# Optimization experiments

Measured on AMD Instinct MI355X. Metric: run time of the kernel, lower is better.

## Reference

```python
import jax, jax.numpy as jnp
import numpy as np

B, S, D, F, T, NS, L, H = 8, 1024, 1024, 4096, 64, 512, 32, 16
TAG_RATE = 0.5      # config.tagging_rate
GSR = 0.5           # config.gate_scaling_rate
ATT_EPS = 1e-12     # config.layer_norm_eps (att_norm)
ENC_EPS = 1e-5      # torch TransformerEncoderLayer default


def _ln(x, g, b, eps):
    m = x.mean(-1, keepdims=True)
    v = x.var(-1, keepdims=True)
    return (x - m) * jax.lax.rsqrt(v + eps) * g + b


def _rope(x):
    # standard rotary embedding over the full hidden dim
    d = x.shape[-1]
    s = x.shape[1]
    inv = 1.0 / (10000.0 ** (jnp.arange(0, d, 2, dtype=jnp.float32) / d))
    ang = jnp.arange(s, dtype=jnp.float32)[:, None] * inv[None, :]  # [S, D/2]
    sin, cos = jnp.sin(ang), jnp.cos(ang)
    x1, x2 = x[..., 0::2], x[..., 1::2]
    return jnp.stack([x1 * cos - x2 * sin, x1 * sin + x2 * cos], axis=-1).reshape(x.shape)


def setup_inputs() -> dict:
    key = jax.random.key(0)
    ks = jax.random.split(key, 24)
    p = lambda k, shp: (0.02 * jax.random.normal(k, shp, dtype=jnp.float32))
    inp = {
        'word_embedding': jax.random.normal(ks[0], (B, S, D), dtype=jnp.float32),
        'attention_mask': jnp.ones((B, S), dtype=jnp.int32),
        'span_batch': jax.random.randint(ks[1], (NS,), 0, B, dtype=jnp.int32),
        'span_start': jax.random.randint(ks[2], (NS,), 0, S - L, dtype=jnp.int32),
        'span_tag': jax.random.randint(ks[3], (NS,), 0, T, dtype=jnp.int32),
        'tag_emb': p(ks[4], (T, D)),
        'gate_w': p(ks[5], (D, 1)),
        'gate_b': jnp.zeros((1,), jnp.float32),
        'attn_ln_g': jnp.ones((D,), jnp.float32),
        'attn_ln_b': jnp.zeros((D,), jnp.float32),
        'in_proj_w': p(ks[6], (3 * D, D)),
        'in_proj_b': jnp.zeros((3 * D,), jnp.float32),
        'out_proj_w': p(ks[7], (D, D)),
        'out_proj_b': jnp.zeros((D,), jnp.float32),
        'enc_ln1_g': jnp.ones((D,), jnp.float32),
        'enc_ln1_b': jnp.zeros((D,), jnp.float32),
        'lin1_w': p(ks[8], (F, D)),
        'lin1_b': jnp.zeros((F,), jnp.float32),
        'lin2_w': p(ks[9], (D, F)),
        'lin2_b': jnp.zeros((D,), jnp.float32),
        'enc_ln2_g': jnp.ones((D,), jnp.float32),
        'enc_ln2_b': jnp.zeros((D,), jnp.float32),
    }
    return inp


def _mha(x, pad, in_proj_w, in_proj_b, out_proj_w, out_proj_b):
    b, s, d = x.shape
    hd = d // H
    qkv = x @ in_proj_w.T + in_proj_b                       # [B,S,3D]
    q, k, v = jnp.split(qkv, 3, axis=-1)
    rs = lambda t: t.reshape(b, s, H, hd).transpose(0, 2, 1, 3)  # [B,H,S,hd]
    q, k, v = rs(q), rs(k), rs(v)
    scores = jnp.einsum('bhqd,bhkd->bhqk', q, k) / jnp.sqrt(jnp.float32(hd))
    scores = jnp.where(pad[:, None, None, :], jnp.float32(-1e30), scores)
    attn = jax.nn.softmax(scores, axis=-1)
    o = jnp.einsum('bhqk,bhkd->bhqd', attn, v).transpose(0, 2, 1, 3).reshape(b, s, d)
    return o @ out_proj_w.T + out_proj_b


def reference(word_embedding, attention_mask, span_batch, span_start, span_tag,
              tag_emb, gate_w, gate_b, attn_ln_g, attn_ln_b,
              in_proj_w, in_proj_b, out_proj_w, out_proj_b,
              enc_ln1_g, enc_ln1_b, lin1_w, lin1_b, lin2_w, lin2_b,
              enc_ln2_g, enc_ln2_b):
    raw = word_embedding                        # dropout off (eval)
    we = _rope(word_embedding)
    # ragged gather -> gate -> scatter-add over fixed-length spans
    tok = span_start[:, None] + jnp.arange(L, dtype=jnp.int32)[None, :]  # [NS,L]
    X = we[span_batch[:, None], tok]            # [NS,L,D]
    gate = GSR * jax.nn.sigmoid(X @ gate_w + gate_b) + (1.0 - GSR) / 2.0  # [NS,L,1]
    res = gate * tag_emb[span_tag][:, None, :] * jnp.float32(L)          # [NS,L,D]
    taged = jnp.zeros_like(word_embedding).at[span_batch[:, None], tok].add(res)
    out_emb = raw + taged * TAG_RATE            # if_merge_by_add
    out_emb = _ln(out_emb, attn_ln_g, attn_ln_b, ATT_EPS)
    pad = attention_mask == 0
    # torch TransformerEncoderLayer (post-norm, relu)
    a = _mha(out_emb, pad, in_proj_w, in_proj_b, out_proj_w, out_proj_b)
    x = _ln(out_emb + a, enc_ln1_g, enc_ln1_b, ENC_EPS)
    ff = jax.nn.relu(x @ lin1_w.T + lin1_b) @ lin2_w.T + lin2_b
    enc = _ln(x + ff, enc_ln2_g, enc_ln2_b, ENC_EPS)
    return enc + out_emb
```

## Files before the change

### kernel.cpp

```cpp
#include <hip/hip_runtime.h>

#define DEV __device__ __forceinline__

typedef short bf16x8 __attribute__((ext_vector_type(8)));
typedef float f32x4 __attribute__((ext_vector_type(4)));
typedef unsigned short u16;
typedef unsigned int u32;

typedef __attribute__((address_space(3))) void lds_void;
typedef __attribute__((address_space(1))) void gbl_void;

DEV void async_copy16(void* lds_dst, const void* g_src) {
    __builtin_amdgcn_global_load_lds((gbl_void*)g_src, (lds_void*)lds_dst, 16, 0, 0);
}

DEV u16 f2bf(float x) {
    u32 u = __float_as_uint(x);
    return (u16)((u + 0x7fffu + ((u >> 16) & 1u)) >> 16);
}
DEV u16 f2bf_fast(float x) {
    return (u16)((__float_as_uint(x) + 0x8000u) >> 16);
}
DEV float bf2f(u16 v) { return __uint_as_float(((u32)v) << 16); }

__global__ __launch_bounds__(256) void f2bf_kernel(const float* __restrict__ src,
                                                   u16* __restrict__ dst, int n4) {
    const int i = blockIdx.x * 256 + threadIdx.x;
    if (i < n4) {
        const float4 v = ((const float4*)src)[i];
        ushort4 o;
        o.x = f2bf(v.x); o.y = f2bf(v.y); o.z = f2bf(v.z); o.w = f2bf(v.w);
        ((ushort4*)dst)[i] = o;
    }
}

__global__ __launch_bounds__(256) void span_kernel(
    const float* __restrict__ we, const int* __restrict__ sb,
    const int* __restrict__ ss, const int* __restrict__ stg,
    const float* __restrict__ tag_emb, const float* __restrict__ gate_w,
    const float* __restrict__ gate_b, float* __restrict__ out_pre) {
    __shared__ float red[4];
    const int n = blockIdx.x >> 5;
    const int l = blockIdx.x & 31;
    const int t = threadIdx.x;
    const int b = sb[n];
    const int s = ss[n] + l;
    const int tag = stg[n];
    const long base = ((long)b * 1024 + s) * 1024;
    float dot = 0.f;
#pragma unroll
    for (int pp = 0; pp < 2; ++pp) {
        const int p = t + pp * 256;
        const float e1 = we[base + 2 * p];
        const float e2 = we[base + 2 * p + 1];
        const float inv = exp2f((float)p * (-13.287712379549449f / 512.0f));
        const float ang = (float)s * inv;
        const float sa = sinf(ang), ca = cosf(ang);
        const float r1 = e1 * ca - e2 * sa;
        const float r2 = e1 * sa + e2 * ca;
        dot += r1 * gate_w[2 * p] + r2 * gate_w[2 * p + 1];
    }
#pragma unroll
    for (int off = 32; off > 0; off >>= 1) dot += __shfl_xor(dot, off, 64);
    if ((t & 63) == 0) red[t >> 6] = dot;
    __syncthreads();
    const float z = red[0] + red[1] + red[2] + red[3] + gate_b[0];
    const float gate = 0.25f + 0.5f / (1.f + __expf(-z));
    const float coef = gate * 16.f;
    const float* te = tag_emb + (long)tag * 1024;
#pragma unroll
    for (int c = 0; c < 4; ++c) {
        const int d = t + c * 256;
        atomicAdd(&out_pre[base + d], coef * te[d]);
    }
}

template <bool WRITE_F32, bool WRITE_BF, bool FINAL>
__global__ __launch_bounds__(256) void ln_kernel(
    const float* __restrict__ X, const float* __restrict__ g,
    const float* __restrict__ bta, float eps, float* __restrict__ Yf,
    u16* __restrict__ Ybf, const u16* __restrict__ addend) {
    __shared__ float red[8];
    const long row = blockIdx.x;
    const int t = threadIdx.x;
    const float4 x = ((const float4*)(X + row * 1024))[t];
    float s = x.x + x.y + x.z + x.w;
#pragma unroll
    for (int off = 32; off > 0; off >>= 1) s += __shfl_xor(s, off, 64);
    if ((t & 63) == 0) red[t >> 6] = s;
    __syncthreads();
    const float mean = (red[0] + red[1] + red[2] + red[3]) * (1.f / 1024.f);
    float4 dx;
    dx.x = x.x - mean; dx.y = x.y - mean; dx.z = x.z - mean; dx.w = x.w - mean;
    float ss = dx.x * dx.x + dx.y * dx.y + dx.z * dx.z + dx.w * dx.w;
#pragma unroll
    for (int off = 32; off > 0; off >>= 1) ss += __shfl_xor(ss, off, 64);
    if ((t & 63) == 0) red[4 + (t >> 6)] = ss;
    __syncthreads();
    const float var = (red[4] + red[5] + red[6] + red[7]) * (1.f / 1024.f);
    const float rstd = rsqrtf(var + eps);
    const float4 gv = ((const float4*)g)[t];
    const float4 bv = ((const float4*)bta)[t];
    float4 y;
    y.x = dx.x * rstd * gv.x + bv.x;
    y.y = dx.y * rstd * gv.y + bv.y;
    y.z = dx.z * rstd * gv.z + bv.z;
    y.w = dx.w * rstd * gv.w + bv.w;
    if (FINAL) {
        const ushort4 a = ((const ushort4*)(addend + row * 1024))[t];
        y.x += bf2f(a.x); y.y += bf2f(a.y); y.z += bf2f(a.z); y.w += bf2f(a.w);
    }
    if (WRITE_F32) ((float4*)(Yf + row * 1024))[t] = y;
    if (WRITE_BF) {
        ushort4 o;
        o.x = f2bf(y.x); o.y = f2bf(y.y); o.z = f2bf(y.z); o.w = f2bf(y.w);
        ((ushort4*)(Ybf + row * 1024))[t] = o;
    }
}

template <bool OUT_BF16, bool RELU, bool HAS_RES>
__global__ __launch_bounds__(256, 2) void gemm_nt(
    const u16* __restrict__ A, const u16* __restrict__ B,
    const float* __restrict__ bias, const u16* __restrict__ res,
    void* __restrict__ Cout, int N, int K) {
    __shared__ u16 Al[4096];
    __shared__ u16 Bl[4096];
    const int tid = threadIdx.x;
    const int wave = tid >> 6;
    const int lane = tid & 63;
    const int quad = lane >> 4;
    const int lq = lane & 15;
    const int wm = wave >> 1;
    const int wn = wave & 1;
    const long rowBase = (long)blockIdx.x * 128;
    const long colBase = (long)blockIdx.y * 128;

    f32x4 acc[4][4];
    const f32x4 fzero = {0.f, 0.f, 0.f, 0.f};
#pragma unroll
    for (int i = 0; i < 4; ++i)
#pragma unroll
        for (int j = 0; j < 4; ++j) acc[i][j] = fzero;

    const int X0 = tid, X1 = 256 + tid;
    const u16* gA0 = A + (rowBase + (X0 >> 2)) * (long)K + (X0 & 3) * 8;
    const u16* gA1 = A + (rowBase + (X1 >> 2)) * (long)K + (X1 & 3) * 8;
    const u16* gB0 = B + (colBase + (X0 >> 2)) * (long)K + (X0 & 3) * 8;
    const u16* gB1 = B + (colBase + (X1 >> 2)) * (long)K + (X1 & 3) * 8;
    u16* lA0 = Al + wave * 512;
    u16* lA1 = Al + 2048 + wave * 512;
    u16* lB0 = Bl + wave * 512;
    u16* lB1 = Bl + 2048 + wave * 512;

    for (int kt = 0; kt < K; kt += 32) {
        __syncthreads();
        async_copy16(lA0, gA0 + kt);
        async_copy16(lA1, gA1 + kt);
        async_copy16(lB0, gB0 + kt);
        async_copy16(lB1, gB1 + kt);
        __syncthreads();
        bf16x8 af[4], bfr[4];
#pragma unroll
        for (int i = 0; i < 4; ++i)
            af[i] = *(const bf16x8*)&Al[(wm * 64 + i * 16 + lq) * 32 + quad * 8];
#pragma unroll
        for (int j = 0; j < 4; ++j)
            bfr[j] = *(const bf16x8*)&Bl[(wn * 64 + j * 16 + lq) * 32 + quad * 8];
#pragma unroll
        for (int i = 0; i < 4; ++i)
#pragma unroll
            for (int j = 0; j < 4; ++j)
                acc[i][j] = __builtin_amdgcn_mfma_f32_16x16x32_bf16(af[i], bfr[j],
                                                                    acc[i][j], 0, 0, 0);
    }

    float biasv[4];
#pragma unroll
    for (int j = 0; j < 4; ++j) biasv[j] = bias[colBase + wn * 64 + j * 16 + lq];
#pragma unroll
    for (int i = 0; i < 4; ++i) {
        const long grow = rowBase + wm * 64 + i * 16 + quad * 4;
#pragma unroll
        for (int j = 0; j < 4; ++j) {
            const long gcol = colBase + wn * 64 + j * 16 + lq;
#pragma unroll
            for (int r = 0; r < 4; ++r) {
                float v = acc[i][j][r] + biasv[j];
                if (RELU) v = fmaxf(v, 0.f);
                if (HAS_RES) v += bf2f(res[(grow + r) * N + gcol]);
                if (OUT_BF16)
                    ((u16*)Cout)[(grow + r) * N + gcol] = f2bf(v);
                else
                    ((float*)Cout)[(grow + r) * N + gcol] = v;
            }
        }
    }
}

__global__ __launch_bounds__(256) void vtrans_kernel(const u16* __restrict__ QKV,
                                                     u16* __restrict__ Vt) {
    __shared__ u16 tile[64][72];
    const int bid = blockIdx.x;
    const int st = bid & 15;
    const int h = (bid >> 4) & 15;
    const int b = bid >> 8;
    const int t = threadIdx.x;
    const int sl = t >> 2;
    const int dc = (t & 3) * 16;
    const u16* src = QKV + ((long)(b * 1024 + st * 64 + sl)) * 3072 + 2048 + h * 64 + dc;
    *(uint4*)&tile[sl][dc] = *(const uint4*)src;
    *(uint4*)&tile[sl][dc + 8] = *(const uint4*)(src + 8);
    __syncthreads();
    const int dl = t >> 2;
    const int sc = (t & 3) * 16;
    union { u16 u[16]; uint4 q[2]; } tmp;
#pragma unroll
    for (int i = 0; i < 16; ++i) tmp.u[i] = tile[sc + i][dl];
    u16* dst = Vt + ((long)(b * 16 + h) * 64 + dl) * 1024 + st * 64 + sc;
    *(uint4*)dst = tmp.q[0];
    *(uint4*)(dst + 8) = tmp.q[1];
}

__global__ __launch_bounds__(256, 4) void attn_kernel(
    const u16* __restrict__ QKV, const u16* __restrict__ Vt,
    const int* __restrict__ mask, u16* __restrict__ Out) {
    __shared__ u16 KL[4096];
    __shared__ u16 VL[4096];
    __shared__ u16 PL[4][16 * 72];
    const int tid = threadIdx.x;
    const int wid = tid >> 6;
    const int lane = tid & 63;
    const int quad = lane >> 4;
    const int lq = lane & 15;
    const int slot0 = quad ^ (lq & 7);
    const int slot1 = slot0 ^ 4;

    const int bid = blockIdx.x;
    const int qb = bid & 7;
    const int h = (bid >> 3) & 15;
    const int b = bid >> 7;
    const int qbase = qb * 128 + wid * 32;

    bf16x8 aq[2][2];
#pragma unroll
    for (int t = 0; t < 2; ++t) {
        const u16* qp = QKV + ((long)(b * 1024 + qbase + t * 16 + lq)) * 3072 +
                        h * 64 + quad * 8;
        aq[t][0] = *(const bf16x8*)qp;
        aq[t][1] = *(const bf16x8*)(qp + 32);
    }

    const int c0 = tid, c1 = 256 + tid;
    const int r0 = c0 >> 3, j0 = (c0 & 7) ^ (r0 & 7);
    const int r1 = c1 >> 3, j1 = (c1 & 7) ^ (r1 & 7);
    const u16* srcK0 = QKV + ((long)(b * 1024 + r0)) * 3072 + 1024 + h * 64 + j0 * 8;
    const u16* srcK1 = QKV + ((long)(b * 1024 + r1)) * 3072 + 1024 + h * 64 + j1 * 8;
    const u16* srcV0 = Vt + ((long)(b * 16 + h) * 64 + r0) * 1024 + j0 * 8;
    const u16* srcV1 = Vt + ((long)(b * 16 + h) * 64 + r1) * 1024 + j1 * 8;
    u16* ldsK0 = KL + wid * 512;
    u16* ldsK1 = KL + 2048 + wid * 512;
    u16* ldsV0 = VL + wid * 512;
    u16* ldsV1 = VL + 2048 + wid * 512;

    const f32x4 fzero = {0.f, 0.f, 0.f, 0.f};
    f32x4 acc[2][4];
#pragma unroll
    for (int t = 0; t < 2; ++t)
#pragma unroll
        for (int j = 0; j < 4; ++j) acc[t][j] = fzero;
    float lsum[2][4] = {{0.f, 0.f, 0.f, 0.f}, {0.f, 0.f, 0.f, 0.f}};
    u16* myP = PL[wid];
    const int* mrow = mask + b * 1024;

    for (int kt = 0; kt < 1024; kt += 64) {
        __syncthreads();
        async_copy16(ldsK0, srcK0 + (long)kt * 3072);
        async_copy16(ldsK1, srcK1 + (long)kt * 3072);
        async_copy16(ldsV0, srcV0 + kt);
        async_copy16(ldsV1, srcV1 + kt);
        __syncthreads();

        bf16x8 kf0[4], kf1[4];
#pragma unroll
        for (int ct = 0; ct < 4; ++ct) {
            const int rowb = (ct * 16 + lq) * 64;
            kf0[ct] = *(const bf16x8*)&KL[rowb + slot0 * 8];
            kf1[ct] = *(const bf16x8*)&KL[rowb + slot1 * 8];
        }
        float mw[4];
#pragma unroll
        for (int ct = 0; ct < 4; ++ct) mw[ct] = mrow[kt + ct * 16 + lq] ? 1.f : 0.f;

#pragma unroll
        for (int t = 0; t < 2; ++t) {
            f32x4 s[4];
#pragma unroll
            for (int ct = 0; ct < 4; ++ct) {
                s[ct] = __builtin_amdgcn_mfma_f32_16x16x32_bf16(aq[t][0], kf0[ct],
                                                                fzero, 0, 0, 0);
                s[ct] = __builtin_amdgcn_mfma_f32_16x16x32_bf16(aq[t][1], kf1[ct],
                                                                s[ct], 0, 0, 0);
            }
            asm volatile("s_waitcnt lgkmcnt(0)" ::: "memory");
#pragma unroll
            for (int ct = 0; ct < 4; ++ct)
#pragma unroll
                for (int r = 0; r < 4; ++r) {
                    const float p = mw[ct] * __expf(s[ct][r] * 0.125f);
                    lsum[t][r] += p;
                    myP[(quad * 4 + r) * 72 + ct * 16 + lq] = f2bf_fast(p);
                }
            asm volatile("s_waitcnt lgkmcnt(0)" ::: "memory");
            const bf16x8 pf0 = *(const bf16x8*)&myP[lq * 72 + quad * 8];
            const bf16x8 pf1 = *(const bf16x8*)&myP[lq * 72 + 32 + quad * 8];
#pragma unroll
            for (int j = 0; j < 4; ++j) {
                const int rowb = (j * 16 + lq) * 64;
                const bf16x8 vf0 = *(const bf16x8*)&VL[rowb + slot0 * 8];
                const bf16x8 vf1 = *(const bf16x8*)&VL[rowb + slot1 * 8];
                acc[t][j] = __builtin_amdgcn_mfma_f32_16x16x32_bf16(pf0, vf0,
                                                                    acc[t][j], 0, 0, 0);
                acc[t][j] = __builtin_amdgcn_mfma_f32_16x16x32_bf16(pf1, vf1,
                                                                    acc[t][j], 0, 0, 0);
            }
        }
    }

#pragma unroll
    for (int t = 0; t < 2; ++t) {
        float inv[4];
#pragma unroll
        for (int r = 0; r < 4; ++r) {
            float l = lsum[t][r];
#pragma unroll
            for (int off = 1; off < 16; off <<= 1) l += __shfl_xor(l, off, 16);
            inv[r] = 1.f / l;
        }
        const long orow = (long)b * 1024 + qbase + t * 16 + quad * 4;
#pragma unroll
        for (int j = 0; j < 4; ++j)
#pragma unroll
            for (int r = 0; r < 4; ++r)
                Out[(orow + r) * 1024 + h * 64 + j * 16 + lq] =
                    f2bf_fast(acc[t][j][r] * inv[r]);
    }
}

extern "C" void kernel_launch(void* const* d_in, const int* in_sizes, int n_in,
                              void* d_out, int out_size, void* d_ws, size_t ws_size,
                              hipStream_t stream) {
    const float* we        = (const float*)d_in[0];
    const int*   amask     = (const int*)d_in[1];
    const int*   span_b    = (const int*)d_in[2];
    const int*   span_s    = (const int*)d_in[3];
    const int*   span_t    = (const int*)d_in[4];
    const float* tag_emb   = (const float*)d_in[5];
    const float* gate_w    = (const float*)d_in[6];
    const float* gate_b    = (const float*)d_in[7];
    const float* attn_ln_g = (const float*)d_in[8];
    const float* attn_ln_b = (const float*)d_in[9];
    const float* in_proj_w = (const float*)d_in[10];
    const float* in_proj_b = (const float*)d_in[11];
    const float* out_proj_w= (const float*)d_in[12];
    const float* out_proj_b= (const float*)d_in[13];
    const float* enc1_g    = (const float*)d_in[14];
    const float* enc1_b    = (const float*)d_in[15];
    const float* lin1_w    = (const float*)d_in[16];
    const float* lin1_b    = (const float*)d_in[17];
    const float* lin2_w    = (const float*)d_in[18];
    const float* lin2_b    = (const float*)d_in[19];
    const float* enc2_g    = (const float*)d_in[20];
    const float* enc2_b    = (const float*)d_in[21];
    float* out = (float*)d_out;

    char* ws = (char*)d_ws;
    size_t off = 0;
    auto alloc = [&](size_t bytes) {
        void* p = ws + off;
        off += (bytes + 255) & ~(size_t)255;
        return p;
    };
    const size_t MT = 8192;
    u16* oe_bf   = (u16*)alloc(MT * 1024 * 2);
    u16* ax_bf   = (u16*)alloc(MT * 1024 * 2);
    char* region = (char*)alloc((size_t)67108864);
    u16* qkv_bf  = (u16*)region;
    u16* vt_bf   = (u16*)(region + (size_t)MT * 3072 * 2);
    u16* ff1_bf  = (u16*)region;
    u16* wb_inproj  = (u16*)alloc((size_t)3072 * 1024 * 2);
    u16* wb_outproj = (u16*)alloc((size_t)1024 * 1024 * 2);
    u16* wb_lin1    = (u16*)alloc((size_t)4096 * 1024 * 2);
    u16* wb_lin2    = (u16*)alloc((size_t)1024 * 4096 * 2);

    hipMemcpyAsync(out, we, MT * 1024 * 4, hipMemcpyDeviceToDevice, stream);
    f2bf_kernel<<<3072, 256, 0, stream>>>(in_proj_w, wb_inproj, 3072 * 1024 / 4);
    f2bf_kernel<<<1024, 256, 0, stream>>>(out_proj_w, wb_outproj, 1024 * 1024 / 4);
    f2bf_kernel<<<4096, 256, 0, stream>>>(lin1_w, wb_lin1, 4096 * 1024 / 4);
    f2bf_kernel<<<4096, 256, 0, stream>>>(lin2_w, wb_lin2, 1024 * 4096 / 4);
    span_kernel<<<16384, 256, 0, stream>>>(we, span_b, span_s, span_t, tag_emb,
                                           gate_w, gate_b, out);
    ln_kernel<false, true, false><<<8192, 256, 0, stream>>>(
        out, attn_ln_g, attn_ln_b, 1e-12f, nullptr, oe_bf, nullptr);
    dim3 g1(64, 24);
    gemm_nt<true, false, false><<<g1, 256, 0, stream>>>(oe_bf, wb_inproj, in_proj_b,
                                                        nullptr, qkv_bf, 3072, 1024);
    vtrans_kernel<<<2048, 256, 0, stream>>>(qkv_bf, vt_bf);
    attn_kernel<<<1024, 256, 0, stream>>>(qkv_bf, vt_bf, amask, ax_bf);
    dim3 g2(64, 8);
    gemm_nt<false, false, true><<<g2, 256, 0, stream>>>(ax_bf, wb_outproj, out_proj_b,
                                                        oe_bf, out, 1024, 1024);
    ln_kernel<false, true, false><<<8192, 256, 0, stream>>>(
        out, enc1_g, enc1_b, 1e-5f, nullptr, ax_bf, nullptr);
    dim3 g3(64, 32);
    gemm_nt<true, true, false><<<g3, 256, 0, stream>>>(ax_bf, wb_lin1, lin1_b,
                                                       nullptr, ff1_bf, 4096, 1024);
    gemm_nt<false, false, true><<<g2, 256, 0, stream>>>(ff1_bf, wb_lin2, lin2_b,
                                                        ax_bf, out, 1024, 4096);
    ln_kernel<true, false, true><<<8192, 256, 0, stream>>>(
        out, enc2_g, enc2_b, 1e-5f, out, nullptr, oe_bf);
}
```

Measured before the change: 596.1 us.

## Switch GEMM to 32x32x16 MFMA with K-tile 64 and fragment-native LDS layout

Rewrites the NT GEMM inner loop to use 32x32x16 bf16 MFMA instructions with 2x2 accumulators per wave instead of 4x4 16x16x32 tiles. The K step is doubled to 64 and the async global-to-LDS copy now lays data out in fragment order, so each lane reads its operand with a contiguous, conflict-free 16-byte load. The aim is fewer LDS reads and fewer barriers per FLOP plus higher MFMA efficiency. The cost is twice the LDS per block, which may lower occupancy, and a reworked epilogue row mapping that must match the 32x32 output layout.

After: 714.0 us. 1.2x slower.

```diff
diff --git a/kernel.cpp b/kernel.cpp
--- a/kernel.cpp
+++ b/kernel.cpp
@@ -4,6 +4,7 @@
 
 typedef short bf16x8 __attribute__((ext_vector_type(8)));
 typedef float f32x4 __attribute__((ext_vector_type(4)));
+typedef float f32x16 __attribute__((ext_vector_type(16)));
 typedef unsigned short u16;
 typedef unsigned int u32;
 
@@ -123,75 +124,76 @@
     const u16* __restrict__ A, const u16* __restrict__ B,
     const float* __restrict__ bias, const u16* __restrict__ res,
     void* __restrict__ Cout, int N, int K) {
-    __shared__ u16 Al[4096];
-    __shared__ u16 Bl[4096];
+    __shared__ u16 Al[8192];
+    __shared__ u16 Bl[8192];
     const int tid = threadIdx.x;
     const int wave = tid >> 6;
     const int lane = tid & 63;
-    const int quad = lane >> 4;
-    const int lq = lane & 15;
+    const int l31 = lane & 31;
+    const int half = lane >> 5;
     const int wm = wave >> 1;
     const int wn = wave & 1;
     const long rowBase = (long)blockIdx.x * 128;
     const long colBase = (long)blockIdx.y * 128;
 
-    f32x4 acc[4][4];
-    const f32x4 fzero = {0.f, 0.f, 0.f, 0.f};
-#pragma unroll
-    for (int i = 0; i < 4; ++i)
-#pragma unroll
-        for (int j = 0; j < 4; ++j) acc[i][j] = fzero;
-
-    const int X0 = tid, X1 = 256 + tid;
-    const u16* gA0 = A + (rowBase + (X0 >> 2)) * (long)K + (X0 & 3) * 8;
-    const u16* gA1 = A + (rowBase + (X1 >> 2)) * (long)K + (X1 & 3) * 8;
-    const u16* gB0 = B + (colBase + (X0 >> 2)) * (long)K + (X0 & 3) * 8;
-    const u16* gB1 = B + (colBase + (X1 >> 2)) * (long)K + (X1 & 3) * 8;
-    u16* lA0 = Al + wave * 512;
-    u16* lA1 = Al + 2048 + wave * 512;
-    u16* lB0 = Bl + wave * 512;
-    u16* lB1 = Bl + 2048 + wave * 512;
-
-    for (int kt = 0; kt < K; kt += 32) {
+    f32x16 acc[2][2];
+#pragma unroll
+    for (int i = 0; i < 2; ++i)
+#pragma unroll
+        for (int j = 0; j < 2; ++j)
+#pragma unroll
+            for (int r = 0; r < 16; ++r) acc[i][j][r] = 0.f;
+
+    const int srow = tid & 31;
+    const int skoff = (tid >> 6) * 16 + ((tid >> 5) & 1) * 8;
+    const u16* gA = A + (rowBase + srow) * (long)K + skoff;
+    const u16* gB = B + (colBase + srow) * (long)K + skoff;
+
+    for (int kt = 0; kt < K; kt += 64) {
         __syncthreads();
-        async_copy16(lA0, gA0 + kt);
-        async_copy16(lA1, gA1 + kt);
-        async_copy16(lB0, gB0 + kt);
-        async_copy16(lB1, gB1 + kt);
+#pragma unroll
+        for (int c = 0; c < 4; ++c) {
+            async_copy16(Al + c * 2048 + wave * 512, gA + (long)c * 32 * K + kt);
+            async_copy16(Bl + c * 2048 + wave * 512, gB + (long)c * 32 * K + kt);
+        }
         __syncthreads();
-        bf16x8 af[4], bfr[4];
-#pragma unroll
-        for (int i = 0; i < 4; ++i)
-            af[i] = *(const bf16x8*)&Al[(wm * 64 + i * 16 + lq) * 32 + quad * 8];
-#pragma unroll
-        for (int j = 0; j < 4; ++j)
-            bfr[j] = *(const bf16x8*)&Bl[(wn * 64 + j * 16 + lq) * 32 + quad * 8];
-#pragma unroll
-        for (int i = 0; i < 4; ++i)
-#pragma unroll
-            for (int j = 0; j < 4; ++j)
-                acc[i][j] = __builtin_amdgcn_mfma_f32_16x16x32_bf16(af[i], bfr[j],
-                                                                    acc[i][j], 0, 0, 0);
-    }
-
-    float biasv[4];
-#pragma unroll
-    for (int j = 0; j < 4; ++j) biasv[j] = bias[colBase + wn * 64 + j * 16 + lq];
-#pragma unroll
-    for (int i = 0; i < 4; ++i) {
-        const long grow = rowBase + wm * 64 + i * 16 + quad * 4;
-#pragma unroll
-        for (int j = 0; j < 4; ++j) {
-            const long gcol = colBase + wn * 64 + j * 16 + lq;
-#pragma unroll
-            for (int r = 0; r < 4; ++r) {
+#pragma unroll
+        for (int ks = 0; ks < 4; ++ks) {
+            bf16x8 af[2], bfr[2];
+#pragma unroll
+            for (int i = 0; i < 2; ++i)
+                af[i] = *(const bf16x8*)&Al[((wm * 2 + i) * 256 + ks * 64 + lane) * 8];
+#pragma unroll
+            for (int j = 0; j < 2; ++j)
+                bfr[j] = *(const bf16x8*)&Bl[((wn * 2 + j) * 256 + ks * 64 + lane) * 8];
+#pragma unroll
+            for (int i = 0; i < 2; ++i)
+#pragma unroll
+                for (int j = 0; j < 2; ++j)
+                    acc[i][j] = __builtin_amdgcn_mfma_f32_32x32x16_bf16(
+                        af[i], bfr[j], acc[i][j], 0, 0, 0);
+        }
+    }
+
+    float biasv[2];
+#pragma unroll
+    for (int j = 0; j < 2; ++j) biasv[j] = bias[colBase + wn * 64 + j * 32 + l31];
+#pragma unroll
+    for (int i = 0; i < 2; ++i) {
+        const long rb = rowBase + wm * 64 + i * 32 + 4 * half;
+#pragma unroll
+        for (int j = 0; j < 2; ++j) {
+            const long gcol = colBase + wn * 64 + j * 32 + l31;
+#pragma unroll
+            for (int r = 0; r < 16; ++r) {
+                const long grow = rb + (r & 3) + 8 * (r >> 2);
                 float v = acc[i][j][r] + biasv[j];
                 if (RELU) v = fmaxf(v, 0.f);
-                if (HAS_RES) v += bf2f(res[(grow + r) * N + gcol]);
+                if (HAS_RES) v += bf2f(res[grow * N + gcol]);
                 if (OUT_BF16)
-                    ((u16*)Cout)[(grow + r) * N + gcol] = f2bf(v);
+                    ((u16*)Cout)[grow * N + gcol] = f2bf(v);
                 else
-                    ((float*)Cout)[(grow + r) * N + gcol] = v;
+                    ((float*)Cout)[grow * N + gcol] = v;
             }
         }
     }
```

## Double GEMM K-tile to 64 and XOR-swizzle LDS layout

Applied to the files above, without the earlier changes.

Raises the GEMM K-step from 32 to 64, so each iteration loads 128x64 tiles of A and B and runs two MFMA sub-steps. This halves the number of barrier pairs per K loop. An XOR swizzle on the 16-byte chunk index is applied to both the global-to-LDS async copy mapping and the fragment reads, to avoid LDS bank conflicts with the wider 64-element rows. The cost is twice the LDS per block (32 KB), which could limit occupancy. There is still no double buffering, so load latency is still exposed on each iteration.

Measured after the change: 542.7 us. 9.0% less time.

```diff
diff --git a/kernel.cpp b/kernel.cpp
--- a/kernel.cpp
+++ b/kernel.cpp
@@ -123,8 +123,8 @@
     const u16* __restrict__ A, const u16* __restrict__ B,
     const float* __restrict__ bias, const u16* __restrict__ res,
     void* __restrict__ Cout, int N, int K) {
-    __shared__ u16 Al[4096];
-    __shared__ u16 Bl[4096];
+    __shared__ u16 Al[8192];
+    __shared__ u16 Bl[8192];
     const int tid = threadIdx.x;
     const int wave = tid >> 6;
     const int lane = tid & 63;
@@ -142,36 +142,41 @@
 #pragma unroll
         for (int j = 0; j < 4; ++j) acc[i][j] = fzero;
 
-    const int X0 = tid, X1 = 256 + tid;
-    const u16* gA0 = A + (rowBase + (X0 >> 2)) * (long)K + (X0 & 3) * 8;
-    const u16* gA1 = A + (rowBase + (X1 >> 2)) * (long)K + (X1 & 3) * 8;
-    const u16* gB0 = B + (colBase + (X0 >> 2)) * (long)K + (X0 & 3) * 8;
-    const u16* gB1 = B + (colBase + (X1 >> 2)) * (long)K + (X1 & 3) * 8;
-    u16* lA0 = Al + wave * 512;
-    u16* lA1 = Al + 2048 + wave * 512;
-    u16* lB0 = Bl + wave * 512;
-    u16* lB1 = Bl + 2048 + wave * 512;
-
-    for (int kt = 0; kt < K; kt += 32) {
+    const int rX = tid >> 3;
+    const int pX = (tid & 7) ^ (rX & 7);
+    const u16* gA = A + (rowBase + rX) * (long)K + pX * 8;
+    const u16* gB = B + (colBase + rX) * (long)K + pX * 8;
+    u16* ldsA = Al + wave * 512;
+    u16* ldsB = Bl + wave * 512;
+
+    for (int kt = 0; kt < K; kt += 64) {
         __syncthreads();
-        async_copy16(lA0, gA0 + kt);
-        async_copy16(lA1, gA1 + kt);
-        async_copy16(lB0, gB0 + kt);
-        async_copy16(lB1, gB1 + kt);
+#pragma unroll
+        for (int c = 0; c < 4; ++c) {
+            async_copy16(ldsA + c * 2048, gA + (long)c * 32 * K + kt);
+            async_copy16(ldsB + c * 2048, gB + (long)c * 32 * K + kt);
+        }
         __syncthreads();
-        bf16x8 af[4], bfr[4];
-#pragma unroll
-        for (int i = 0; i < 4; ++i)
-            af[i] = *(const bf16x8*)&Al[(wm * 64 + i * 16 + lq) * 32 + quad * 8];
-#pragma unroll
-        for (int j = 0; j < 4; ++j)
-            bfr[j] = *(const bf16x8*)&Bl[(wn * 64 + j * 16 + lq) * 32 + quad * 8];
-#pragma unroll
-        for (int i = 0; i < 4; ++i)
-#pragma unroll
-            for (int j = 0; j < 4; ++j)
-                acc[i][j] = __builtin_amdgcn_mfma_f32_16x16x32_bf16(af[i], bfr[j],
-                                                                    acc[i][j], 0, 0, 0);
+#pragma unroll
+        for (int ks = 0; ks < 2; ++ks) {
+            bf16x8 af[4], bfr[4];
+#pragma unroll
+            for (int i = 0; i < 4; ++i) {
+                const int r = wm * 64 + i * 16 + lq;
+                af[i] = *(const bf16x8*)&Al[r * 64 + (((ks * 4 + quad) ^ (lq & 7)) * 8)];
+            }
+#pragma unroll
+            for (int j = 0; j < 4; ++j) {
+                const int r = wn * 64 + j * 16 + lq;
+                bfr[j] = *(const bf16x8*)&Bl[r * 64 + (((ks * 4 + quad) ^ (lq & 7)) * 8)];
+            }
+#pragma unroll
+            for (int i = 0; i < 4; ++i)
+#pragma unroll
+                for (int j = 0; j < 4; ++j)
+                    acc[i][j] = __builtin_amdgcn_mfma_f32_16x16x32_bf16(
+                        af[i], bfr[j], acc[i][j], 0, 0, 0);
+        }
     }
 
     float biasv[4];
```
